# Optimization experiments

Hardware: AMD Instinct MI355X
Metric: run time of the kernel (lower is better)

The kernel has to match this reference:

```python
import jax, jax.numpy as jnp
import numpy as np


def setup_inputs() -> dict:
    key = jax.random.key(0)
    kx, kw = jax.random.split(key)
    x = jax.random.normal(kx, (32, 256, 56, 56), dtype=jnp.float32)
    # kaiming-uniform-like init for weights [O, I, K, K]
    fan_in = 256 * 3 * 3
    bound = float(np.sqrt(6.0 / fan_in))
    weights = jax.random.uniform(kw, (256, 256, 3, 3), dtype=jnp.float32,
                                 minval=-bound, maxval=bound)
    return {"x": x, "weights": weights}


def reference(x, weights):
    # Binarize weights with sign (STE is a backward-only concern; forward uses sign).
    qw = jnp.sign(weights)
    # conv2d, NCHW / OIHW, stride 1, no padding, no bias
    out = jax.lax.conv_general_dilated(
        x, qw,
        window_strides=(1, 1),
        padding="VALID",
        dimension_numbers=("NCHW", "OIHW", "NCHW"),
    )
    return out
```

## Files before the change

kernel.cpp:

```cpp
#include <hip/hip_runtime.h>
#include <cstdint>

#define NB 32
#define IC 256
#define OC 256
#define H 56
#define WIDTH 56
#define OH 54
#define OW 54
#define HW (H*WIDTH)
#define OHW (OH*OW)
#define KTOT 2304
#define M_TOT (NB*OHW)
#define C8N (IC/8)

#define BM 128
#define BO 256
#define BK 32
#define KSTEPS (KTOT/BK)
#define MBLOCKS (M_TOT/BM)

__device__ __align__(16) unsigned short g_qwt[KSTEPS*BO*BK];
__device__ __align__(16) unsigned short g_xq[NB*C8N*HW*8];

typedef __bf16 bf16x8 __attribute__((ext_vector_type(8)));
typedef float  f32x4  __attribute__((ext_vector_type(4)));

typedef __attribute__((address_space(1))) const unsigned int gas_u32;
typedef __attribute__((address_space(3))) unsigned int las_u32;
__device__ __forceinline__ void async_copy16(const void* g, void* l) {
  __builtin_amdgcn_global_load_lds((gas_u32*)g, (las_u32*)l, 16, 0, 0);
}

__device__ inline unsigned short f32_bf16(float f) {
  union { float f; unsigned int u; } v; v.f = f;
  unsigned int u = v.u;
  return (unsigned short)((u + 0x7FFFu + ((u >> 16) & 1u)) >> 16);
}

__global__ __launch_bounds__(256) void repack_w(const float* __restrict__ w) {
  int L = blockIdx.x * 256 + threadIdx.x;
  int step = L >> 13;
  int r    = (L >> 5) & 255;
  int kc   = L & 31;
  int cs   = kc >> 3;
  int b    = kc & 7;
  int csrc = cs ^ ((r >> 1) & 3);
  int k    = step*BK + csrc*8 + b;
  int pos  = k >> 8;
  int c    = k & 255;
  float v = w[r*2304 + c*9 + pos];
  unsigned short s = (v > 0.f) ? 0x3F80u : ((v < 0.f) ? 0xBF80u : 0u);
  g_qwt[L] = s;
}

__global__ __launch_bounds__(256) void xform_x(const float* __restrict__ x) {
  int g = blockIdx.x * 256 + threadIdx.x;
  int hw = g % HW;
  int tc = g / HW;
  int c8 = tc & 31;
  int n  = tc >> 5;
  const float* src = x + (n*IC + c8*8)*HW + hw;
  unsigned int o[4];
  #pragma unroll
  for (int j = 0; j < 4; ++j) {
    unsigned int lo = f32_bf16(src[(2*j+0)*HW]);
    unsigned int hi = f32_bf16(src[(2*j+1)*HW]);
    o[j] = lo | (hi << 16);
  }
  *(uint4*)(&g_xq[g*8]) = *(uint4*)o;
}

__global__ __launch_bounds__(512, 4) void bconv_gemm(float* __restrict__ out) {
  __shared__ __align__(16) unsigned short Wl[2][BO*BK];
  __shared__ __align__(16) unsigned short Xl[2][BM*BK];
  const int t = threadIdx.x;

  const int orig = blockIdx.x;
  const int xcd  = orig & 7;
  const int idx  = orig >> 3;
  const int bm   = (xcd == 0) ? idx : (92 + (xcd - 1)*91 + idx);
  const int m0   = bm * BM;

  int xbase;
  {
    const int i   = t >> 2;
    const int cs  = t & 3;
    const int csw = cs ^ ((i >> 1) & 3);
    int m  = m0 + i;
    int n  = m / OHW;
    int rm = m - n*OHW;
    int oh = rm / OW;
    int ow = rm - oh*OW;
    xbase = ((n*C8N + csw)*HW + oh*WIDTH + ow) * 8;
  }

  const int lane = t & 63;
  const int wv   = t >> 6;
  const int col  = lane & 15;
  const int quad = lane >> 4;
  const int wo   = (wv >> 1) * 64;
  const int wm   = (wv & 1) * 64;
  const int sw   = (quad ^ ((col >> 1) & 3)) * 8;
  int aoff[4], boff[4];
  #pragma unroll
  for (int i = 0; i < 4; ++i) {
    aoff[i] = (wo + i*16 + col)*BK + sw;
    boff[i] = (wm + i*16 + col)*BK + sw;
  }

  auto STAGE = [&](int step, int buf) {
    const unsigned short* ws = g_qwt + step*(BO*BK);
    async_copy16(&ws[t*8],       &Wl[buf][t*8]);
    async_copy16(&ws[(t+512)*8], &Wl[buf][(t+512)*8]);
    const int pos = step >> 3;
    const int kh  = pos / 3;
    const int kw  = pos - kh*3;
    const int xo  = xbase + (((step & 7)*4)*HW + kh*WIDTH + kw)*8;
    async_copy16(&g_xq[xo], &Xl[buf][t*8]);
  };

  f32x4 acc[4][4];
  #pragma unroll
  for (int a = 0; a < 4; ++a)
    #pragma unroll
    for (int b = 0; b < 4; ++b)
      acc[a][b] = (f32x4){0.f, 0.f, 0.f, 0.f};

  STAGE(0, 0);
  __syncthreads();
  int cur = 0;
  for (int step = 0; step < KSTEPS; ++step) {
    if (step + 1 < KSTEPS) STAGE(step + 1, cur ^ 1);

    bf16x8 av[4], bv[4];
    #pragma unroll
    for (int i = 0; i < 4; ++i) av[i] = *(const bf16x8*)(&Wl[cur][aoff[i]]);
    #pragma unroll
    for (int i = 0; i < 4; ++i) bv[i] = *(const bf16x8*)(&Xl[cur][boff[i]]);

    #pragma unroll
    for (int io = 0; io < 4; ++io)
      #pragma unroll
      for (int im = 0; im < 4; ++im)
        acc[io][im] = __builtin_amdgcn_mfma_f32_16x16x32_bf16(av[io], bv[im], acc[io][im], 0, 0, 0);

    __syncthreads();
    cur ^= 1;
  }

  #pragma unroll
  for (int im = 0; im < 4; ++im) {
    int m  = m0 + wm + im*16 + col;
    int n  = m / OHW;
    int rm = m - n*OHW;
    float* obase = out + n*(OC*OHW) + rm;
    #pragma unroll
    for (int io = 0; io < 4; ++io) {
      int orow = wo + io*16 + quad*4;
      #pragma unroll
      for (int r = 0; r < 4; ++r)
        obase[(orow + r)*OHW] = acc[io][im][r];
    }
  }
}

extern "C" void kernel_launch(void* const* d_in, const int* in_sizes, int n_in,
                              void* d_out, int out_size, void* d_ws, size_t ws_size,
                              hipStream_t stream) {
  const float* x = (const float*)d_in[0];
  const float* w = (const float*)d_in[1];
  float* out = (float*)d_out;

  repack_w<<<dim3((KSTEPS*BO*BK)/256), 256, 0, stream>>>(w);
  xform_x <<<dim3((NB*C8N*HW)/256), 256, 0, stream>>>(x);
  bconv_gemm<<<dim3(MBLOCKS), 512, 0, stream>>>(out);
}
```

Baseline: 338.0 us.

## Triple-buffer LDS staging with explicit vmcnt waits and MFMA priority

Replaces the double-buffered K loop with a three-stage LDS ring, so two global-to-LDS async copies stay in flight while one stage is computed. Explicit s_waitcnt vmcnt counts and sched-barrier-fenced s_barriers replace the __syncthreads calls, and s_setprio raises wave priority around the MFMA block. The aim is to hide global load latency better behind the matrix math. The cost is a larger LDS footprint per block, which can cut the number of resident blocks per CU.

```diff
diff --git a/kernel.cpp b/kernel.cpp
--- a/kernel.cpp
+++ b/kernel.cpp
@@ -37,6 +37,13 @@
   unsigned int u = v.u;
   return (unsigned short)((u + 0x7FFFu + ((u >> 16) & 1u)) >> 16);
 }
+
+#define WAITV(N) asm volatile("s_waitcnt vmcnt(" #N ")" ::: "memory")
+#define BARRIER() do { \
+  __builtin_amdgcn_sched_barrier(0); \
+  __builtin_amdgcn_s_barrier(); \
+  __builtin_amdgcn_sched_barrier(0); \
+} while (0)
 
 __global__ __launch_bounds__(256) void repack_w(const float* __restrict__ w) {
   int L = blockIdx.x * 256 + threadIdx.x;
@@ -72,8 +79,8 @@
 }
 
 __global__ __launch_bounds__(512, 4) void bconv_gemm(float* __restrict__ out) {
-  __shared__ __align__(16) unsigned short Wl[2][BO*BK];
-  __shared__ __align__(16) unsigned short Xl[2][BM*BK];
+  __shared__ __align__(16) unsigned short Wl[3][BO*BK];
+  __shared__ __align__(16) unsigned short Xl[3][BM*BK];
   const int t = threadIdx.x;
 
   const int orig = blockIdx.x;
@@ -127,27 +134,57 @@
     for (int b = 0; b < 4; ++b)
       acc[a][b] = (f32x4){0.f, 0.f, 0.f, 0.f};
 
-  STAGE(0, 0);
-  __syncthreads();
-  int cur = 0;
-  for (int step = 0; step < KSTEPS; ++step) {
-    if (step + 1 < KSTEPS) STAGE(step + 1, cur ^ 1);
-
+  auto COMPUTE = [&](const unsigned short* Wb, const unsigned short* Xb) {
     bf16x8 av[4], bv[4];
     #pragma unroll
-    for (int i = 0; i < 4; ++i) av[i] = *(const bf16x8*)(&Wl[cur][aoff[i]]);
-    #pragma unroll
-    for (int i = 0; i < 4; ++i) bv[i] = *(const bf16x8*)(&Xl[cur][boff[i]]);
-
+    for (int i = 0; i < 4; ++i) av[i] = *(const bf16x8*)(&Wb[aoff[i]]);
+    #pragma unroll
+    for (int i = 0; i < 4; ++i) bv[i] = *(const bf16x8*)(&Xb[boff[i]]);
+    __builtin_amdgcn_s_setprio(1);
     #pragma unroll
     for (int io = 0; io < 4; ++io)
       #pragma unroll
       for (int im = 0; im < 4; ++im)
         acc[io][im] = __builtin_amdgcn_mfma_f32_16x16x32_bf16(av[io], bv[im], acc[io][im], 0, 0, 0);
-
-    __syncthreads();
-    cur ^= 1;
-  }
+    __builtin_amdgcn_s_setprio(0);
+  };
+
+  STAGE(0, 0);
+  STAGE(1, 1);
+  STAGE(2, 2);
+  WAITV(6);
+  BARRIER();
+  COMPUTE(Wl[0], Xl[0]);
+
+  #pragma unroll 1
+  for (int s = 1; s < 68; s += 3) {
+    BARRIER();
+    STAGE(s + 2, 0);
+    WAITV(6);
+    BARRIER();
+    COMPUTE(Wl[1], Xl[1]);
+
+    BARRIER();
+    STAGE(s + 3, 1);
+    WAITV(6);
+    BARRIER();
+    COMPUTE(Wl[2], Xl[2]);
+
+    BARRIER();
+    STAGE(s + 4, 2);
+    WAITV(6);
+    BARRIER();
+    COMPUTE(Wl[0], Xl[0]);
+  }
+
+  BARRIER();
+  WAITV(3);
+  BARRIER();
+  COMPUTE(Wl[1], Xl[1]);
+  BARRIER();
+  WAITV(0);
+  BARRIER();
+  COMPUTE(Wl[2], Xl[2]);
 
   #pragma unroll
   for (int im = 0; im < 4; ++im) {
```

Result: faster. 312.3 us (-7.6%).
